# Kernel tuning notes

Measured on AMD Instinct MI355X. Metric: run time of the kernel, lower is better.

Reference implementation:

```python
import jax, jax.numpy as jnp
import numpy as np

H = 16          # ATTENTION_HEAD
E = 300         # EXPANSION_LENGTH
D = 768         # TEXT_EMBEDDING_DIM
HD = D // H     # 48


def setup_inputs() -> dict:
    key = jax.random.key(0)
    ks = jax.random.split(key, 10)
    b, n, ql, kl = 1, 4, 64, 64
    q = jax.random.normal(ks[0], (b, n, ql, D), dtype=jnp.float32)
    k = jax.random.normal(ks[1], (b, 1, kl, D), dtype=jnp.float32)
    v = jax.random.normal(ks[2], (b, 1, kl, D), dtype=jnp.float32)
    s = 1.0 / np.sqrt(D)
    Wq = jax.random.normal(ks[3], (D, D), dtype=jnp.float32) * s
    bq = jnp.zeros((D,), dtype=jnp.float32)
    Wk = jax.random.normal(ks[4], (D, D), dtype=jnp.float32) * s
    bk = jnp.zeros((D,), dtype=jnp.float32)
    Wv = jax.random.normal(ks[5], (D, D), dtype=jnp.float32) * s
    bv = jnp.zeros((D,), dtype=jnp.float32)
    memory = jax.random.normal(ks[6], (1, E, H, HD), dtype=jnp.float32) * 0.05
    return {"q": q, "k": k, "v": v, "Wq": Wq, "bq": bq, "Wk": Wk,
            "bk": bk, "Wv": Wv, "bv": bv, "memory": memory}


def reference(q, k, v, Wq, bq, Wk, bk, Wv, bv, memory):
    b, n, ql, _ = q.shape
    kl = k.shape[2]
    # Dense projections
    Q = (q @ Wq + bq).reshape(b, n, ql, H, HD)          # bnqhd
    K = (k @ Wk + bk).reshape(b, kl, H, HD)             # bkhd
    V = (v @ Wv + bv).reshape(b, kl, H, HD)             # bkhd
    # memory (1,E,H,HD) -> (1,E,1,H,HD); K -> (b,1,kl,H,HD); broadcast sum
    broad_sum = memory[:, :, None, :, :] + K[:, None, :, :, :]   # bekhd
    M = jax.nn.relu(jnp.einsum('bekhd,bnqhd->bnekqh', broad_sum, Q))
    E_seq = jnp.einsum('bnekqh,bkhd->bnekhd', M, V)
    out = jnp.einsum('bnekhd,bnekqh->bnqhd', E_seq, M)
    return out.reshape(q.shape)
```

## Files before the change

### kernel.cpp

```cpp
#include <hip/hip_runtime.h>

#define H   16
#define E   300
#define D   768
#define HD  48
#define QL  64
#define KL  64
#define NH  64
#define ROWS 384
#define SPLITK 12
#define NEG 8
#define ECH 38

#define OFF_PP 0
#define OFF_PF (SPLITK*ROWS*D)
#define OFF_OP (OFF_PF + ROWS*D)

__global__ __launch_bounds__(256, 2) void proj_kernel(
    const float* __restrict__ qin, const float* __restrict__ kin, const float* __restrict__ vin,
    const float* __restrict__ Wq, const float* __restrict__ Wk, const float* __restrict__ Wv,
    float* __restrict__ ws)
{
    const int rowblk = blockIdx.x;
    const int col0   = blockIdx.y * 128;
    const int ks     = blockIdx.z;
    const int kbase  = ks * 64;

    const float* W = (rowblk < 4) ? Wq : (rowblk == 4) ? Wk : Wv;

    __shared__ float XsT[32][68];
    __shared__ float Ws[32][128];

    const int tid = threadIdx.x;
    const int r0  = (tid >> 4) * 4;
    const int c0  = (tid & 15) * 8;

    float acc[4][8];
    #pragma unroll
    for (int i = 0; i < 4; i++)
        #pragma unroll
        for (int j = 0; j < 8; j++) acc[i][j] = 0.f;

    for (int kk2 = 0; kk2 < 64; kk2 += 32) {
        #pragma unroll
        for (int it = 0; it < 2; it++) {
            const int idx = it * 256 + tid;
            const int row = idx >> 3;
            const int d4  = (idx & 7) * 4;
            const int grow = rowblk * 64 + row;
            const float* src = (grow < 256) ? (qin + grow * D)
                             : (grow < 320) ? (kin + (grow - 256) * D)
                                            : (vin + (grow - 320) * D);
            const float4 xv = *(const float4*)(src + kbase + kk2 + d4);
            XsT[d4 + 0][row] = xv.x; XsT[d4 + 1][row] = xv.y;
            XsT[d4 + 2][row] = xv.z; XsT[d4 + 3][row] = xv.w;
        }
        #pragma unroll
        for (int it = 0; it < 4; it++) {
            const int idx = it * 256 + tid;
            const int dk  = idx >> 5;
            const int c4  = (idx & 31) * 4;
            *(float4*)&Ws[dk][c4] =
                *(const float4*)(W + (kbase + kk2 + dk) * D + col0 + c4);
        }
        __syncthreads();
        #pragma unroll
        for (int dk = 0; dk < 32; dk++) {
            const float4 x0 = *(const float4*)&XsT[dk][r0];
            const float4 w0 = *(const float4*)&Ws[dk][c0];
            const float4 w1 = *(const float4*)&Ws[dk][c0 + 4];
            const float xr[4] = {x0.x, x0.y, x0.z, x0.w};
            const float wc[8] = {w0.x, w0.y, w0.z, w0.w, w1.x, w1.y, w1.z, w1.w};
            #pragma unroll
            for (int i = 0; i < 4; i++)
                #pragma unroll
                for (int j = 0; j < 8; j++)
                    acc[i][j] = fmaf(xr[i], wc[j], acc[i][j]);
        }
        __syncthreads();
    }
    float* P = ws + OFF_PP + ks * (ROWS * D);
    #pragma unroll
    for (int i = 0; i < 4; i++) {
        float* base = P + (rowblk * 64 + r0 + i) * D + col0 + c0;
        *(float4*)(base)     = make_float4(acc[i][0], acc[i][1], acc[i][2], acc[i][3]);
        *(float4*)(base + 4) = make_float4(acc[i][4], acc[i][5], acc[i][6], acc[i][7]);
    }
}

__global__ __launch_bounds__(256) void reduce_kernel(
    const float* __restrict__ bq, const float* __restrict__ bk, const float* __restrict__ bv,
    float* __restrict__ ws)
{
    const int idx = (blockIdx.x * 256 + threadIdx.x) * 4;
    const float* PP = ws + OFF_PP;
    float4 v = *(const float4*)(PP + idx);
    #pragma unroll
    for (int c = 1; c < SPLITK; c++) {
        const float4 p = *(const float4*)(PP + c * (ROWS * D) + idx);
        v.x += p.x; v.y += p.y; v.z += p.z; v.w += p.w;
    }
    const int row = idx / D, col = idx % D;
    const float* bias = (row < 256) ? bq : (row < 320) ? bk : bv;
    const float4 b = *(const float4*)(bias + col);
    v.x += b.x; v.y += b.y; v.z += b.z; v.w += b.w;
    *(float4*)(ws + OFF_PF + idx) = v;
}

__global__ __launch_bounds__(256, 2) void mega_kernel(
    const float* __restrict__ memo, float* __restrict__ ws)
{
    const int nh = blockIdx.x;
    const int eg = blockIdx.y;
    const int e0 = eg * ECH;
    const int ecnt = (E - e0 < ECH) ? (E - e0) : ECH;
    const int n = nh >> 4, h = nh & 15;
    const int tid = threadIdx.x;
    const int lane = tid & 63;
    const int w = tid >> 6;

    const float* Pf = ws + OFF_PF;

    __shared__ float As[ECH * 64];
    __shared__ float Bs[64][68];
    __shared__ float U[8832];

    float* QsT = U;
    float* KsT = U + 48 * 68;
    float* MsT = U + 2 * 48 * 68;

    #pragma unroll
    for (int it = 0; it < 3; it++) {
        const int idx = it * 256 + tid;
        const int r  = idx / 12;
        const int d4 = (idx % 12) * 4;
        const float4 qv = *(const float4*)(Pf + (n * QL + r) * D + h * HD + d4);
        QsT[(d4 + 0) * 68 + r] = qv.x; QsT[(d4 + 1) * 68 + r] = qv.y;
        QsT[(d4 + 2) * 68 + r] = qv.z; QsT[(d4 + 3) * 68 + r] = qv.w;
        const float4 kv = *(const float4*)(Pf + (256 + r) * D + h * HD + d4);
        KsT[(d4 + 0) * 68 + r] = kv.x; KsT[(d4 + 1) * 68 + r] = kv.y;
        KsT[(d4 + 2) * 68 + r] = kv.z; KsT[(d4 + 3) * 68 + r] = kv.w;
    }
    for (int idx = tid; idx < ecnt * 12; idx += 256) {
        const int e  = idx / 12;
        const int d4 = (idx % 12) * 4;
        const float4 mv = *(const float4*)(memo + (e0 + e) * D + h * HD + d4);
        MsT[(d4 + 0) * 40 + e] = mv.x; MsT[(d4 + 1) * 40 + e] = mv.y;
        MsT[(d4 + 2) * 40 + e] = mv.z; MsT[(d4 + 3) * 40 + e] = mv.w;
    }
    __syncthreads();

    {
        const int k0 = (tid >> 4) * 4;
        const int q0 = (tid & 15) * 4;
        float acc[4][4];
        #pragma unroll
        for (int i = 0; i < 4; i++)
            #pragma unroll
            for (int j = 0; j < 4; j++) acc[i][j] = 0.f;
        #pragma unroll 4
        for (int d = 0; d < HD; d++) {
            const float4 kf = *(const float4*)&KsT[d * 68 + k0];
            const float4 qf = *(const float4*)&QsT[d * 68 + q0];
            const float kk4[4] = {kf.x, kf.y, kf.z, kf.w};
            const float qq4[4] = {qf.x, qf.y, qf.z, qf.w};
            #pragma unroll
            for (int i = 0; i < 4; i++)
                #pragma unroll
                for (int j = 0; j < 4; j++)
                    acc[i][j] = fmaf(kk4[i], qq4[j], acc[i][j]);
        }
        #pragma unroll
        for (int i = 0; i < 4; i++)
            *(float4*)&Bs[k0 + i][q0] =
                make_float4(acc[i][0], acc[i][1], acc[i][2], acc[i][3]);
    }
    {
        const int et = (tid >> 4) * 3;
        const int q0 = (tid & 15) * 4;
        float acc[3][4];
        #pragma unroll
        for (int i = 0; i < 3; i++)
            #pragma unroll
            for (int j = 0; j < 4; j++) acc[i][j] = 0.f;
        #pragma unroll 4
        for (int d = 0; d < HD; d++) {
            const float me0 = MsT[d * 40 + et + 0];
            const float me1 = MsT[d * 40 + et + 1];
            const float me2 = MsT[d * 40 + et + 2];
            const float4 qf = *(const float4*)&QsT[d * 68 + q0];
            const float mm3[3] = {me0, me1, me2};
            const float qq4[4] = {qf.x, qf.y, qf.z, qf.w};
            #pragma unroll
            for (int i = 0; i < 3; i++)
                #pragma unroll
                for (int j = 0; j < 4; j++)
                    acc[i][j] = fmaf(mm3[i], qq4[j], acc[i][j]);
        }
        #pragma unroll
        for (int i = 0; i < 3; i++)
            if (et + i < ecnt)
                *(float4*)&As[(et + i) * 64 + q0] =
                    make_float4(acc[i][0], acc[i][1], acc[i][2], acc[i][3]);
    }
    __syncthreads();

    float b[64];
    #pragma unroll
    for (int j = 0; j < 16; j++)
        *(float4*)&b[j * 4] = *(const float4*)&Bs[lane][j * 4];
    __syncthreads();

    float* Vs = &Bs[0][0];
    #pragma unroll
    for (int it = 0; it < 3; it++) {
        const int idx = it * 256 + tid;
        const int k  = idx / 12;
        const int d4 = (idx % 12) * 4;
        const float4 vv = *(const float4*)(Pf + (320 + k) * D + h * HD + d4);
        *(float4*)&Vs[k * 52 + d4] = vv;
    }

    float s[64];
    #pragma unroll
    for (int j = 0; j < 64; j++) s[j] = 0.f;

    const int eBeg = (ecnt * w) >> 2;
    const int eEnd = (ecnt * (w + 1)) >> 2;
    for (int e = eBeg; e < eEnd; e++) {
        float m[64];
        #pragma unroll
        for (int j4 = 0; j4 < 16; j4++) {
            const float4 a = *(const float4*)&As[e * 64 + j4 * 4];
            m[j4 * 4 + 0] = fmaxf(a.x + b[j4 * 4 + 0], 0.f);
            m[j4 * 4 + 1] = fmaxf(a.y + b[j4 * 4 + 1], 0.f);
            m[j4 * 4 + 2] = fmaxf(a.z + b[j4 * 4 + 2], 0.f);
            m[j4 * 4 + 3] = fmaxf(a.w + b[j4 * 4 + 3], 0.f);
        }
        float p0 = 0.f, p1 = 0.f, p2 = 0.f, p3 = 0.f;
        #pragma unroll
        for (int j4 = 0; j4 < 16; j4++) {
            p0 += m[j4 * 4 + 0]; p1 += m[j4 * 4 + 1];
            p2 += m[j4 * 4 + 2]; p3 += m[j4 * 4 + 3];
        }
        const float p = (p0 + p1) + (p2 + p3);
        #pragma unroll
        for (int j = 0; j < 64; j++)
            s[j] = fmaf(m[j], p, s[j]);
    }

    float* r0 = U;
    float* r1 = U + 4096;
    float* Ss = U + 4096;
    __syncthreads();
    if (w >= 2) {
        float* red = (w == 2) ? r0 : r1;
        #pragma unroll
        for (int q = 0; q < 64; q++) red[q * 64 + lane] = s[q];
    }
    __syncthreads();
    if (w == 0) {
        #pragma unroll
        for (int q = 0; q < 64; q++) s[q] += r0[q * 64 + lane];
    } else if (w == 1) {
        #pragma unroll
        for (int q = 0; q < 64; q++) s[q] += r1[q * 64 + lane];
    }
    __syncthreads();
    if (w == 1) {
        #pragma unroll
        for (int q = 0; q < 64; q++) r0[q * 64 + lane] = s[q];
    }
    __syncthreads();
    if (w == 0) {
        #pragma unroll
        for (int q = 0; q < 64; q++)
            Ss[q * 68 + lane] = s[q] + r0[q * 64 + lane];
    }
    __syncthreads();

    {
        const int q  = tid >> 2;
        const int dg = tid & 3;
        float4 a0 = make_float4(0.f, 0.f, 0.f, 0.f);
        float4 a1 = a0, a2 = a0;
        #pragma unroll 8
        for (int k = 0; k < KL; k++) {
            const float sv = Ss[q * 68 + k];
            const float4 v0 = *(const float4*)&Vs[k * 52 + dg * 12 + 0];
            const float4 v1 = *(const float4*)&Vs[k * 52 + dg * 12 + 4];
            const float4 v2 = *(const float4*)&Vs[k * 52 + dg * 12 + 8];
            a0.x = fmaf(sv, v0.x, a0.x); a0.y = fmaf(sv, v0.y, a0.y);
            a0.z = fmaf(sv, v0.z, a0.z); a0.w = fmaf(sv, v0.w, a0.w);
            a1.x = fmaf(sv, v1.x, a1.x); a1.y = fmaf(sv, v1.y, a1.y);
            a1.z = fmaf(sv, v1.z, a1.z); a1.w = fmaf(sv, v1.w, a1.w);
            a2.x = fmaf(sv, v2.x, a2.x); a2.y = fmaf(sv, v2.y, a2.y);
            a2.z = fmaf(sv, v2.z, a2.z); a2.w = fmaf(sv, v2.w, a2.w);
        }
        float* OP = ws + OFF_OP + (((eg * NH) + nh) * QL + q) * 48 + dg * 12;
        *(float4*)(OP + 0) = a0;
        *(float4*)(OP + 4) = a1;
        *(float4*)(OP + 8) = a2;
    }
}

__global__ __launch_bounds__(256) void outsum_kernel(
    const float* __restrict__ ws_c, float* __restrict__ outp)
{
    const int g = blockIdx.x * 256 + threadIdx.x;
    const int d12 = g % 12;
    const int q   = (g / 12) & 63;
    const int nh  = g / 768;
    const int n = nh >> 4, h = nh & 15;
    const float* OP = ws_c + OFF_OP;

    float4 acc = make_float4(0.f, 0.f, 0.f, 0.f);
    #pragma unroll
    for (int c = 0; c < NEG; c++) {
        const float4 p = *(const float4*)(OP + c * (NH * QL * 48)
                                          + (nh * QL + q) * 48 + d12 * 4);
        acc.x += p.x; acc.y += p.y; acc.z += p.z; acc.w += p.w;
    }
    *(float4*)(outp + (n * QL + q) * D + h * HD + d12 * 4) = acc;
}

extern "C" void kernel_launch(void* const* d_in, const int* in_sizes, int n_in,
                              void* d_out, int out_size, void* d_ws, size_t ws_size,
                              hipStream_t stream)
{
    const float* q    = (const float*)d_in[0];
    const float* k    = (const float*)d_in[1];
    const float* v    = (const float*)d_in[2];
    const float* Wq   = (const float*)d_in[3];
    const float* bq   = (const float*)d_in[4];
    const float* Wk   = (const float*)d_in[5];
    const float* bk   = (const float*)d_in[6];
    const float* Wv   = (const float*)d_in[7];
    const float* bv   = (const float*)d_in[8];
    const float* memo = (const float*)d_in[9];
    float* ws   = (float*)d_ws;
    float* outp = (float*)d_out;

    hipLaunchKernelGGL(proj_kernel, dim3(6, 6, 12), dim3(256), 0, stream,
                       q, k, v, Wq, Wk, Wv, ws);
    hipLaunchKernelGGL(reduce_kernel, dim3(288), dim3(256), 0, stream, bq, bk, bv, ws);
    hipLaunchKernelGGL(mega_kernel, dim3(64, NEG), dim3(256), 0, stream, memo, ws);
    hipLaunchKernelGGL(outsum_kernel, dim3(192), dim3(256), 0, stream, ws, outp);
}
```

Before: 117.0 us.

## Drop split-K projection reduce and fuse output sum into mega kernel

The projection kernel now accumulates over the full K dimension per block with smaller 32x64 tiles and adds the bias itself, so the separate split-K reduce kernel and its partial-sum traffic go away. The final reduction over the e-chunks moves into mega_kernel: each block takes a ticket from a per-head atomic counter, and the last block for that head sums the partials and writes the output. This removes two kernel launches and the round trips through workspace memory between them. In exchange the projection has less parallelism and lower per-thread arithmetic intensity, and correctness depends on the ticket counters starting at a multiple of 8, since nothing resets them.

```diff
diff --git a/kernel.cpp b/kernel.cpp
--- a/kernel.cpp
+++ b/kernel.cpp
@@ -8,107 +8,86 @@
 #define KL  64
 #define NH  64
 #define ROWS 384
-#define SPLITK 12
 #define NEG 8
 #define ECH 38
 
-#define OFF_PP 0
-#define OFF_PF (SPLITK*ROWS*D)
-#define OFF_OP (OFF_PF + ROWS*D)
-
-__global__ __launch_bounds__(256, 2) void proj_kernel(
+#define OFF_PF 0
+#define OFF_OP (ROWS*D)
+#define OFF_TICK (OFF_OP + NEG*NH*QL*48)
+
+__global__ __launch_bounds__(256, 2) void projPf_kernel(
     const float* __restrict__ qin, const float* __restrict__ kin, const float* __restrict__ vin,
     const float* __restrict__ Wq, const float* __restrict__ Wk, const float* __restrict__ Wv,
+    const float* __restrict__ bq, const float* __restrict__ bk, const float* __restrict__ bv,
     float* __restrict__ ws)
 {
-    const int rowblk = blockIdx.x;
-    const int col0   = blockIdx.y * 128;
-    const int ks     = blockIdx.z;
-    const int kbase  = ks * 64;
-
-    const float* W = (rowblk < 4) ? Wq : (rowblk == 4) ? Wk : Wv;
-
-    __shared__ float XsT[32][68];
-    __shared__ float Ws[32][128];
+    const int bx = blockIdx.x;
+    const int by = blockIdx.y;
+
+    const float* W    = (bx < 8) ? Wq : (bx < 10) ? Wk : Wv;
+    const float* bias = (bx < 8) ? bq : (bx < 10) ? bk : bv;
+
+    __shared__ float XsT[64][36];
+    __shared__ float Ws[64][64];
 
     const int tid = threadIdx.x;
-    const int r0  = (tid >> 4) * 4;
-    const int c0  = (tid & 15) * 8;
-
-    float acc[4][8];
-    #pragma unroll
-    for (int i = 0; i < 4; i++)
-        #pragma unroll
-        for (int j = 0; j < 8; j++) acc[i][j] = 0.f;
-
-    for (int kk2 = 0; kk2 < 64; kk2 += 32) {
+    const int r0  = (tid >> 5) * 4;
+    const int c0  = (tid & 31) * 2;
+
+    float acc[4][2];
+    #pragma unroll
+    for (int i = 0; i < 4; i++) { acc[i][0] = 0.f; acc[i][1] = 0.f; }
+
+    for (int kb = 0; kb < D; kb += 64) {
         #pragma unroll
         for (int it = 0; it < 2; it++) {
             const int idx = it * 256 + tid;
-            const int row = idx >> 3;
-            const int d4  = (idx & 7) * 4;
-            const int grow = rowblk * 64 + row;
+            const int row = idx >> 4;
+            const int d4  = (idx & 15) * 4;
+            const int grow = bx * 32 + row;
             const float* src = (grow < 256) ? (qin + grow * D)
                              : (grow < 320) ? (kin + (grow - 256) * D)
                                             : (vin + (grow - 320) * D);
-            const float4 xv = *(const float4*)(src + kbase + kk2 + d4);
+            const float4 xv = *(const float4*)(src + kb + d4);
             XsT[d4 + 0][row] = xv.x; XsT[d4 + 1][row] = xv.y;
             XsT[d4 + 2][row] = xv.z; XsT[d4 + 3][row] = xv.w;
         }
         #pragma unroll
         for (int it = 0; it < 4; it++) {
             const int idx = it * 256 + tid;
-            const int dk  = idx >> 5;
-            const int c4  = (idx & 31) * 4;
+            const int dk  = idx >> 4;
+            const int c4  = (idx & 15) * 4;
             *(float4*)&Ws[dk][c4] =
-                *(const float4*)(W + (kbase + kk2 + dk) * D + col0 + c4);
+                *(const float4*)(W + (kb + dk) * D + by * 64 + c4);
         }
         __syncthreads();
-        #pragma unroll
-        for (int dk = 0; dk < 32; dk++) {
-            const float4 x0 = *(const float4*)&XsT[dk][r0];
-            const float4 w0 = *(const float4*)&Ws[dk][c0];
-            const float4 w1 = *(const float4*)&Ws[dk][c0 + 4];
-            const float xr[4] = {x0.x, x0.y, x0.z, x0.w};
-            const float wc[8] = {w0.x, w0.y, w0.z, w0.w, w1.x, w1.y, w1.z, w1.w};
-            #pragma unroll
-            for (int i = 0; i < 4; i++)
-                #pragma unroll
-                for (int j = 0; j < 8; j++)
-                    acc[i][j] = fmaf(xr[i], wc[j], acc[i][j]);
+        #pragma unroll 16
+        for (int dk = 0; dk < 64; dk++) {
+            const float4 x4 = *(const float4*)&XsT[dk][r0];
+            const float2 w2 = *(const float2*)&Ws[dk][c0];
+            acc[0][0] = fmaf(x4.x, w2.x, acc[0][0]);
+            acc[0][1] = fmaf(x4.x, w2.y, acc[0][1]);
+            acc[1][0] = fmaf(x4.y, w2.x, acc[1][0]);
+            acc[1][1] = fmaf(x4.y, w2.y, acc[1][1]);
+            acc[2][0] = fmaf(x4.z, w2.x, acc[2][0]);
+            acc[2][1] = fmaf(x4.z, w2.y, acc[2][1]);
+            acc[3][0] = fmaf(x4.w, w2.x, acc[3][0]);
+            acc[3][1] = fmaf(x4.w, w2.y, acc[3][1]);
         }
         __syncthreads();
     }
-    float* P = ws + OFF_PP + ks * (ROWS * D);
+    const int colg = by * 64 + c0;
+    const float2 bb = *(const float2*)(bias + colg);
+    float* Pf = ws + OFF_PF;
     #pragma unroll
     for (int i = 0; i < 4; i++) {
-        float* base = P + (rowblk * 64 + r0 + i) * D + col0 + c0;
-        *(float4*)(base)     = make_float4(acc[i][0], acc[i][1], acc[i][2], acc[i][3]);
-        *(float4*)(base + 4) = make_float4(acc[i][4], acc[i][5], acc[i][6], acc[i][7]);
+        const float2 out = make_float2(acc[i][0] + bb.x, acc[i][1] + bb.y);
+        *(float2*)(Pf + (bx * 32 + r0 + i) * D + colg) = out;
     }
 }
 
-__global__ __launch_bounds__(256) void reduce_kernel(
-    const float* __restrict__ bq, const float* __restrict__ bk, const float* __restrict__ bv,
-    float* __restrict__ ws)
-{
-    const int idx = (blockIdx.x * 256 + threadIdx.x) * 4;
-    const float* PP = ws + OFF_PP;
-    float4 v = *(const float4*)(PP + idx);
-    #pragma unroll
-    for (int c = 1; c < SPLITK; c++) {
-        const float4 p = *(const float4*)(PP + c * (ROWS * D) + idx);
-        v.x += p.x; v.y += p.y; v.z += p.z; v.w += p.w;
-    }
-    const int row = idx / D, col = idx % D;
-    const float* bias = (row < 256) ? bq : (row < 320) ? bk : bv;
-    const float4 b = *(const float4*)(bias + col);
-    v.x += b.x; v.y += b.y; v.z += b.z; v.w += b.w;
-    *(float4*)(ws + OFF_PF + idx) = v;
-}
-
 __global__ __launch_bounds__(256, 2) void mega_kernel(
-    const float* __restrict__ memo, float* __restrict__ ws)
+    const float* __restrict__ memo, float* __restrict__ ws, float* __restrict__ outp)
 {
     const int nh = blockIdx.x;
     const int eg = blockIdx.y;
@@ -124,6 +103,7 @@
     __shared__ float As[ECH * 64];
     __shared__ float Bs[64][68];
     __shared__ float U[8832];
+    __shared__ int winner;
 
     float* QsT = U;
     float* KsT = U + 48 * 68;
@@ -302,26 +282,37 @@
         *(float4*)(OP + 4) = a1;
         *(float4*)(OP + 8) = a2;
     }
-}
-
-__global__ __launch_bounds__(256) void outsum_kernel(
-    const float* __restrict__ ws_c, float* __restrict__ outp)
-{
-    const int g = blockIdx.x * 256 + threadIdx.x;
-    const int d12 = g % 12;
-    const int q   = (g / 12) & 63;
-    const int nh  = g / 768;
-    const int n = nh >> 4, h = nh & 15;
-    const float* OP = ws_c + OFF_OP;
-
-    float4 acc = make_float4(0.f, 0.f, 0.f, 0.f);
-    #pragma unroll
-    for (int c = 0; c < NEG; c++) {
-        const float4 p = *(const float4*)(OP + c * (NH * QL * 48)
-                                          + (nh * QL + q) * 48 + d12 * 4);
-        acc.x += p.x; acc.y += p.y; acc.z += p.z; acc.w += p.w;
-    }
-    *(float4*)(outp + (n * QL + q) * D + h * HD + d12 * 4) = acc;
+
+    __syncthreads();
+    if (tid == 0) {
+        unsigned* tick = (unsigned*)(ws + OFF_TICK);
+        const unsigned old = __hip_atomic_fetch_add(&tick[nh], 1u,
+                                 __ATOMIC_ACQ_REL, __HIP_MEMORY_SCOPE_AGENT);
+        winner = ((old & 7u) == 7u) ? 1 : 0;
+    }
+    __syncthreads();
+    if (winner) {
+        __threadfence();
+        const int q  = tid >> 2;
+        const int dg = tid & 3;
+        const float* OP = ws + OFF_OP;
+        float4 a0 = make_float4(0.f, 0.f, 0.f, 0.f);
+        float4 a1 = a0, a2 = a0;
+        #pragma unroll
+        for (int c = 0; c < NEG; c++) {
+            const float* src = OP + ((c * NH + nh) * QL + q) * 48 + dg * 12;
+            const float4 p0 = *(const float4*)(src + 0);
+            const float4 p1 = *(const float4*)(src + 4);
+            const float4 p2 = *(const float4*)(src + 8);
+            a0.x += p0.x; a0.y += p0.y; a0.z += p0.z; a0.w += p0.w;
+            a1.x += p1.x; a1.y += p1.y; a1.z += p1.z; a1.w += p1.w;
+            a2.x += p2.x; a2.y += p2.y; a2.z += p2.z; a2.w += p2.w;
+        }
+        float* dst = outp + (n * QL + q) * D + h * HD + dg * 12;
+        *(float4*)(dst + 0) = a0;
+        *(float4*)(dst + 4) = a1;
+        *(float4*)(dst + 8) = a2;
+    }
 }
 
 extern "C" void kernel_launch(void* const* d_in, const int* in_sizes, int n_in,
@@ -341,9 +332,8 @@
     float* ws   = (float*)d_ws;
     float* outp = (float*)d_out;
 
-    hipLaunchKernelGGL(proj_kernel, dim3(6, 6, 12), dim3(256), 0, stream,
-                       q, k, v, Wq, Wk, Wv, ws);
-    hipLaunchKernelGGL(reduce_kernel, dim3(288), dim3(256), 0, stream, bq, bk, bv, ws);
-    hipLaunchKernelGGL(mega_kernel, dim3(64, NEG), dim3(256), 0, stream, memo, ws);
-    hipLaunchKernelGGL(outsum_kernel, dim3(192), dim3(256), 0, stream, ws, outp);
+    hipLaunchKernelGGL(projPf_kernel, dim3(12, 12), dim3(256), 0, stream,
+                       q, k, v, Wq, Wk, Wv, bq, bk, bv, ws);
+    hipLaunchKernelGGL(mega_kernel, dim3(64, NEG), dim3(256), 0, stream,
+                       memo, ws, outp);
 }
```

After: 146.9 us. 25.5% more time.
